# Performance work log

Measured on AMD Instinct MI355X. Metric: run time of the kernel, lower is better.

Reference implementation:

```python
import jax, jax.numpy as jnp
import numpy as np

B, L, H, I = 2, 2048, 4096, 11008


def setup_inputs() -> dict:
    key = jax.random.key(0)
    k1, k2, k3, k4, k5 = jax.random.split(key, 5)
    s_h = 1.0 / np.sqrt(H)
    s_i = 1.0 / np.sqrt(I)
    return {
        "hidden_states": jax.random.normal(k1, (B, L, H), dtype=jnp.float32),
        "w_up": jax.random.normal(k2, (I, H), dtype=jnp.float32) * s_h,
        "w_gate": jax.random.normal(k3, (I, H), dtype=jnp.float32) * s_h,
        "w_down": jax.random.normal(k4, (H, I), dtype=jnp.float32) * s_i,
        "route_mask": jax.random.randint(k5, (B, L), 0, 2, dtype=jnp.int32),
    }


def reference(hidden_states, w_up, w_gate, w_down, route_mask):
    # M-axis (per-token) route-masked gated MLP (SwiGLU, no biases).
    # up/gate: [B,L,H] @ [H,I] -> [B,L,I]; down: [B,L,I] @ [I,H] -> [B,L,H]
    up = jnp.einsum("blh,ih->bli", hidden_states, w_up)
    gate = jax.nn.silu(jnp.einsum("blh,ih->bli", hidden_states, w_gate))
    m = route_mask.astype(hidden_states.dtype)[..., None]  # [B,L,1]
    h = up * gate * m  # masked tokens contribute zero (down has no bias)
    return jnp.einsum("bli,hi->blh", h, w_down)
```

## Files before the change

kernel.cpp:

```cpp
#include <hip/hip_runtime.h>
#include <stdint.h>

#define MB_ 2
#define LL_ 2048
#define M_ (MB_*LL_)
#define H_ 4096
#define I_ 11008

typedef __attribute__((ext_vector_type(8))) short bf16x8;
typedef __attribute__((ext_vector_type(4))) float f32x4;
typedef __attribute__((ext_vector_type(4))) unsigned short us4;

__device__ __forceinline__ unsigned short f2bf(float f) {
  union { float f; unsigned int u; } v; v.f = f;
  unsigned int r = v.u + 0x7FFFu + ((v.u >> 16) & 1u);
  return (unsigned short)(r >> 16);
}

__device__ __forceinline__ void gl2lds16(const void* g, void* l) {
  __builtin_amdgcn_global_load_lds(
      (const __attribute__((address_space(1))) void*)g,
      (__attribute__((address_space(3))) void*)l, 16, 0, 0);
}

#define WAITV4 asm volatile("s_waitcnt vmcnt(4)" ::: "memory")
#define WAITV0 asm volatile("s_waitcnt vmcnt(0)" ::: "memory")
#define BAR    __builtin_amdgcn_s_barrier()

__global__ __launch_bounds__(256)
void compact_mask(const int* __restrict__ mask, int* __restrict__ idx,
                  int* __restrict__ cnt) {
  __shared__ int lcnt[256];
  __shared__ int loff[256];
  __shared__ int stot;
  const int t = threadIdx.x;
  const int base = t * 16;
  int c = 0;
#pragma unroll
  for (int j = 0; j < 16; j++) c += (mask[base + j] != 0);
  lcnt[t] = c;
  __syncthreads();
  if (t == 0) {
    int s = 0;
    for (int i = 0; i < 256; i++) { loff[i] = s; s += lcnt[i]; }
    stot = s;
    cnt[0] = s;
  }
  __syncthreads();
  int o = loff[t];
#pragma unroll
  for (int j = 0; j < 16; j++)
    if (mask[base + j] != 0) idx[o++] = base + j;
  const int total = stot;
  for (int s = total + t; s < M_; s += 256) idx[s] = 0;
}

__global__ __launch_bounds__(256)
void cvt_bf16(const float* __restrict__ src, unsigned short* __restrict__ dst, int n8) {
  int i = blockIdx.x * blockDim.x + threadIdx.x;
  if (i >= n8) return;
  const float4* s = (const float4*)src + (size_t)i * 2;
  float4 a = s[0], b = s[1];
  us4 lo = { f2bf(a.x), f2bf(a.y), f2bf(a.z), f2bf(a.w) };
  us4 hi = { f2bf(b.x), f2bf(b.y), f2bf(b.z), f2bf(b.w) };
  us4* d = (us4*)dst + (size_t)i * 2;
  d[0] = lo; d[1] = hi;
}

__global__ __launch_bounds__(256)
void gather_cvt_hs(const float* __restrict__ hs, const int* __restrict__ idx,
                   unsigned short* __restrict__ dst) {
  const int slot = blockIdx.x;
  const int row  = idx[slot];
  const int col  = (blockIdx.y * 256 + threadIdx.x) * 8;
  const float4* s = (const float4*)(hs + (size_t)row * H_ + col);
  float4 a = s[0], b = s[1];
  us4 lo = { f2bf(a.x), f2bf(a.y), f2bf(a.z), f2bf(a.w) };
  us4 hi = { f2bf(b.x), f2bf(b.y), f2bf(b.z), f2bf(b.w) };
  unsigned short* d = dst + (size_t)slot * H_ + col;
  *(us4*)d = lo;
  *(us4*)(d + 4) = hi;
}

__global__ __launch_bounds__(256)
void mlp_upgate3(const unsigned short* __restrict__ hs16c,
                 const unsigned short* __restrict__ wu16,
                 const unsigned short* __restrict__ wg16,
                 const int* __restrict__ cnt,
                 unsigned short* __restrict__ hbuf)
{
  const int mtiles = (cnt[0] + 127) >> 7;

  const int lin = blockIdx.y * 32 + blockIdx.x;
  const int sw  = (lin & 7) * 688 + (lin >> 3);
  const int mt  = sw & 31;
  const int nt  = sw >> 5;
  if (mt >= mtiles) return;

  __shared__ unsigned short As[3][128 * 32];
  __shared__ unsigned short Bu[3][64 * 32];
  __shared__ unsigned short Bg[3][64 * 32];

  const int tid  = threadIdx.x;
  const int m0   = mt * 128;
  const int n0   = nt * 64;
  const int w    = tid >> 6;
  const int lane = tid & 63;
  const int quad = lane >> 4;
  const int rrow = lane & 15;
  const int wm   = (w & 1) * 64;
  const int wn   = (w >> 1) * 32;

  const int lr = lane >> 2;
  const int lc = (lane & 3) * 8;
  const unsigned short* pa0 = hs16c + (size_t)(m0 + w * 32 + lr) * H_ + lc;
  const unsigned short* pa1 = pa0 + (size_t)16 * H_;
  const unsigned short* pu  = wu16 + (size_t)(n0 + w * 16 + lr) * H_ + lc;
  const unsigned short* pg  = wg16 + (size_t)(n0 + w * 16 + lr) * H_ + lc;

  auto stage = [&](int t, int b) {
    const int k0 = t * 32;
    gl2lds16(pa0 + k0, &As[b][(w * 32) * 32]);
    gl2lds16(pa1 + k0, &As[b][(w * 32 + 16) * 32]);
    gl2lds16(pu  + k0, &Bu[b][(w * 16) * 32]);
    gl2lds16(pg  + k0, &Bg[b][(w * 16) * 32]);
  };

  f32x4 accU[4][2], accG[4][2];
  const f32x4 zero = {0.f, 0.f, 0.f, 0.f};
  for (int i = 0; i < 4; i++)
    for (int j = 0; j < 2; j++) { accU[i][j] = zero; accG[i][j] = zero; }

  const int NT = H_ / 32;
  stage(0, 0);
  stage(1, 1);
  WAITV4;
  BAR;

  int b = 0, bs = 2;
  for (int t = 0; t < NT; ++t) {
    if (t + 2 < NT) stage(t + 2, bs);
    bf16x8 af[4], bu[2], bg[2];
#pragma unroll
    for (int mi = 0; mi < 4; mi++)
      af[mi] = *(const bf16x8*)&As[b][(wm + mi * 16 + rrow) * 32 + quad * 8];
#pragma unroll
    for (int ni = 0; ni < 2; ni++) {
      bu[ni] = *(const bf16x8*)&Bu[b][(wn + ni * 16 + rrow) * 32 + quad * 8];
      bg[ni] = *(const bf16x8*)&Bg[b][(wn + ni * 16 + rrow) * 32 + quad * 8];
    }
#pragma unroll
    for (int mi = 0; mi < 4; mi++)
#pragma unroll
      for (int ni = 0; ni < 2; ni++) {
        accU[mi][ni] = __builtin_amdgcn_mfma_f32_16x16x32_bf16(af[mi], bu[ni], accU[mi][ni], 0, 0, 0);
        accG[mi][ni] = __builtin_amdgcn_mfma_f32_16x16x32_bf16(af[mi], bg[ni], accG[mi][ni], 0, 0, 0);
      }
    if (t + 2 < NT) { WAITV4; } else { WAITV0; }
    BAR;
    b  = (b  + 1 == 3) ? 0 : b  + 1;
    bs = (bs + 1 == 3) ? 0 : bs + 1;
  }

#pragma unroll
  for (int mi = 0; mi < 4; mi++)
#pragma unroll
    for (int ni = 0; ni < 2; ni++)
#pragma unroll
      for (int r = 0; r < 4; r++) {
        int row = wm + mi * 16 + quad * 4 + r;
        int col = wn + ni * 16 + rrow;
        float u = accU[mi][ni][r];
        float g = accG[mi][ni][r];
        float sig = 1.0f / (1.0f + __expf(-g));
        hbuf[(size_t)(m0 + row) * I_ + n0 + col] = f2bf(u * g * sig);
      }
}

__global__ __launch_bounds__(256)
void mlp_down3(const unsigned short* __restrict__ hbuf,
               const unsigned short* __restrict__ wd16,
               const int* __restrict__ idx, const int* __restrict__ cnt,
               float* __restrict__ out)
{
  const int count  = cnt[0];
  const int mtiles = (count + 127) >> 7;

  const int lin = blockIdx.y * 32 + blockIdx.x;
  const int sw  = (lin & 7) * 128 + (lin >> 3);
  const int mt  = sw & 31;
  const int nt  = sw >> 5;
  if (mt >= mtiles) return;

  __shared__ unsigned short As[3][128 * 32];
  __shared__ unsigned short Bs[3][128 * 32];

  const int tid  = threadIdx.x;
  const int m0   = mt * 128;
  const int n0   = nt * 128;
  const int w    = tid >> 6;
  const int lane = tid & 63;
  const int quad = lane >> 4;
  const int rrow = lane & 15;
  const int wm   = (w & 1) * 64;
  const int wn   = (w >> 1) * 64;

  const int lr = lane >> 2;
  const int lc = (lane & 3) * 8;
  const unsigned short* pa0 = hbuf + (size_t)(m0 + w * 32 + lr) * I_ + lc;
  const unsigned short* pa1 = pa0 + (size_t)16 * I_;
  const unsigned short* pb0 = wd16 + (size_t)(n0 + w * 32 + lr) * I_ + lc;
  const unsigned short* pb1 = pb0 + (size_t)16 * I_;

  auto stage = [&](int t, int b) {
    const int k0 = t * 32;
    gl2lds16(pa0 + k0, &As[b][(w * 32) * 32]);
    gl2lds16(pa1 + k0, &As[b][(w * 32 + 16) * 32]);
    gl2lds16(pb0 + k0, &Bs[b][(w * 32) * 32]);
    gl2lds16(pb1 + k0, &Bs[b][(w * 32 + 16) * 32]);
  };

  f32x4 acc[4][4];
  const f32x4 zero = {0.f, 0.f, 0.f, 0.f};
  for (int i = 0; i < 4; i++)
    for (int j = 0; j < 4; j++) acc[i][j] = zero;

  const int NT = I_ / 32;
  stage(0, 0);
  stage(1, 1);
  WAITV4;
  BAR;

  int b = 0, bs = 2;
  for (int t = 0; t < NT; ++t) {
    if (t + 2 < NT) stage(t + 2, bs);
    bf16x8 af[4], bf[4];
#pragma unroll
    for (int mi = 0; mi < 4; mi++)
      af[mi] = *(const bf16x8*)&As[b][(wm + mi * 16 + rrow) * 32 + quad * 8];
#pragma unroll
    for (int ni = 0; ni < 4; ni++)
      bf[ni] = *(const bf16x8*)&Bs[b][(wn + ni * 16 + rrow) * 32 + quad * 8];
#pragma unroll
    for (int mi = 0; mi < 4; mi++)
#pragma unroll
      for (int ni = 0; ni < 4; ni++)
        acc[mi][ni] = __builtin_amdgcn_mfma_f32_16x16x32_bf16(af[mi], bf[ni], acc[mi][ni], 0, 0, 0);
    if (t + 2 < NT) { WAITV4; } else { WAITV0; }
    BAR;
    b  = (b  + 1 == 3) ? 0 : b  + 1;
    bs = (bs + 1 == 3) ? 0 : bs + 1;
  }

#pragma unroll
  for (int mi = 0; mi < 4; mi++)
#pragma unroll
    for (int r = 0; r < 4; r++) {
      int row  = wm + mi * 16 + quad * 4 + r;
      int slot = m0 + row;
      if (slot < count) {
        int tok = idx[slot];
        float* orow = out + (size_t)tok * H_ + n0;
#pragma unroll
        for (int ni = 0; ni < 4; ni++)
          orow[wn + ni * 16 + rrow] = acc[mi][ni][r];
      }
    }
}

#define TM 128
#define TN 128
#define BK 32
#define LDK 40

__global__ __launch_bounds__(256)
void mlp_upgate_fb(const float* __restrict__ hs, const float* __restrict__ wu,
                   const float* __restrict__ wg, const int* __restrict__ mask,
                   unsigned short* __restrict__ hbuf)
{
  __shared__ unsigned short As[TM * LDK];
  __shared__ unsigned short Bu[TN * LDK];
  __shared__ unsigned short Bg[TN * LDK];
  __shared__ float smask[TM];

  const int tid = threadIdx.x;
  const int m0 = blockIdx.x * TM;
  const int n0 = blockIdx.y * TN;
  if (tid < TM) smask[tid] = (float)mask[m0 + tid];
  const int wave = tid >> 6, lane = tid & 63;
  const int quad = lane >> 4, rrow = lane & 15;
  const int wm = (wave & 1) * 64, wn = (wave >> 1) * 64;

  f32x4 accU[4][4], accG[4][4];
  const f32x4 zero = {0.f, 0.f, 0.f, 0.f};
  for (int i = 0; i < 4; i++)
    for (int j = 0; j < 4; j++) { accU[i][j] = zero; accG[i][j] = zero; }

  for (int k0 = 0; k0 < H_; k0 += BK) {
#pragma unroll
    for (int s = 0; s < 4; s++) {
      int idx2 = tid + s * 256, row = idx2 >> 3, c4 = (idx2 & 7) * 4;
      float4 a = *(const float4*)&hs[(size_t)(m0 + row) * H_ + k0 + c4];
      float4 u = *(const float4*)&wu[(size_t)(n0 + row) * H_ + k0 + c4];
      float4 g = *(const float4*)&wg[(size_t)(n0 + row) * H_ + k0 + c4];
      us4 av = { f2bf(a.x), f2bf(a.y), f2bf(a.z), f2bf(a.w) };
      us4 uv = { f2bf(u.x), f2bf(u.y), f2bf(u.z), f2bf(u.w) };
      us4 gv = { f2bf(g.x), f2bf(g.y), f2bf(g.z), f2bf(g.w) };
      *(us4*)&As[row * LDK + c4] = av;
      *(us4*)&Bu[row * LDK + c4] = uv;
      *(us4*)&Bg[row * LDK + c4] = gv;
    }
    __syncthreads();
    bf16x8 af[4], bu[4], bg[4];
#pragma unroll
    for (int mi = 0; mi < 4; mi++)
      af[mi] = *(const bf16x8*)&As[(wm + mi * 16 + rrow) * LDK + quad * 8];
#pragma unroll
    for (int ni = 0; ni < 4; ni++) {
      bu[ni] = *(const bf16x8*)&Bu[(wn + ni * 16 + rrow) * LDK + quad * 8];
      bg[ni] = *(const bf16x8*)&Bg[(wn + ni * 16 + rrow) * LDK + quad * 8];
    }
#pragma unroll
    for (int mi = 0; mi < 4; mi++)
#pragma unroll
      for (int ni = 0; ni < 4; ni++) {
        accU[mi][ni] = __builtin_amdgcn_mfma_f32_16x16x32_bf16(af[mi], bu[ni], accU[mi][ni], 0, 0, 0);
        accG[mi][ni] = __builtin_amdgcn_mfma_f32_16x16x32_bf16(af[mi], bg[ni], accG[mi][ni], 0, 0, 0);
      }
    __syncthreads();
  }
#pragma unroll
  for (int mi = 0; mi < 4; mi++)
#pragma unroll
    for (int ni = 0; ni < 4; ni++)
#pragma unroll
      for (int r = 0; r < 4; r++) {
        int row = wm + mi * 16 + quad * 4 + r;
        int col = wn + ni * 16 + rrow;
        float u = accU[mi][ni][r], g = accG[mi][ni][r];
        float sig = 1.0f / (1.0f + __expf(-g));
        hbuf[(size_t)(m0 + row) * I_ + n0 + col] = f2bf(u * g * sig * smask[row]);
      }
}

__global__ __launch_bounds__(256)
void mlp_down_fb(const unsigned short* __restrict__ hbuf,
                 const float* __restrict__ wd, float* __restrict__ out)
{
  __shared__ unsigned short As[TM * LDK];
  __shared__ unsigned short Bs[TN * LDK];
  const int tid = threadIdx.x;
  const int m0 = blockIdx.x * TM, n0 = blockIdx.y * TN;
  const int wave = tid >> 6, lane = tid & 63;
  const int quad = lane >> 4, rrow = lane & 15;
  const int wm = (wave & 1) * 64, wn = (wave >> 1) * 64;

  f32x4 acc[4][4];
  const f32x4 zero = {0.f, 0.f, 0.f, 0.f};
  for (int i = 0; i < 4; i++)
    for (int j = 0; j < 4; j++) acc[i][j] = zero;

  for (int k0 = 0; k0 < I_; k0 += BK) {
#pragma unroll
    for (int s = 0; s < 4; s++) {
      int idx2 = tid + s * 256, row = idx2 >> 3, c4 = (idx2 & 7) * 4;
      us4 av = *(const us4*)&hbuf[(size_t)(m0 + row) * I_ + k0 + c4];
      float4 b = *(const float4*)&wd[(size_t)(n0 + row) * I_ + k0 + c4];
      us4 bv = { f2bf(b.x), f2bf(b.y), f2bf(b.z), f2bf(b.w) };
      *(us4*)&As[row * LDK + c4] = av;
      *(us4*)&Bs[row * LDK + c4] = bv;
    }
    __syncthreads();
    bf16x8 af[4], bf[4];
#pragma unroll
    for (int mi = 0; mi < 4; mi++)
      af[mi] = *(const bf16x8*)&As[(wm + mi * 16 + rrow) * LDK + quad * 8];
#pragma unroll
    for (int ni = 0; ni < 4; ni++)
      bf[ni] = *(const bf16x8*)&Bs[(wn + ni * 16 + rrow) * LDK + quad * 8];
#pragma unroll
    for (int mi = 0; mi < 4; mi++)
#pragma unroll
      for (int ni = 0; ni < 4; ni++)
        acc[mi][ni] = __builtin_amdgcn_mfma_f32_16x16x32_bf16(af[mi], bf[ni], acc[mi][ni], 0, 0, 0);
    __syncthreads();
  }
#pragma unroll
  for (int mi = 0; mi < 4; mi++)
#pragma unroll
    for (int ni = 0; ni < 4; ni++)
#pragma unroll
      for (int r = 0; r < 4; r++) {
        int row = wm + mi * 16 + quad * 4 + r;
        int col = wn + ni * 16 + rrow;
        out[(size_t)(m0 + row) * H_ + n0 + col] = acc[mi][ni][r];
      }
}

extern "C" void kernel_launch(void* const* d_in, const int* in_sizes, int n_in,
                              void* d_out, int out_size, void* d_ws, size_t ws_size,
                              hipStream_t stream) {
  const float* hs  = (const float*)d_in[0];
  const float* wu  = (const float*)d_in[1];
  const float* wg  = (const float*)d_in[2];
  const float* wd  = (const float*)d_in[3];
  const int*   msk = (const int*)d_in[4];
  float* out = (float*)d_out;

  const size_t SZ_H  = (size_t)M_ * I_ * 2;
  const size_t SZ_HS = (size_t)M_ * H_ * 2;
  const size_t SZ_W  = (size_t)I_ * H_ * 2;
  const size_t SZ_IDX = (size_t)M_ * 4 + 64;
  const size_t NEED = SZ_H + SZ_HS + 3 * SZ_W + SZ_IDX;

  unsigned short* hbuf = (unsigned short*)d_ws;

  if (ws_size >= NEED) {
    char* p = (char*)d_ws;
    unsigned short* hs16c = (unsigned short*)(p + SZ_H);
    unsigned short* wu16  = (unsigned short*)(p + SZ_H + SZ_HS);
    unsigned short* wg16  = (unsigned short*)(p + SZ_H + SZ_HS + SZ_W);
    unsigned short* wd16  = (unsigned short*)(p + SZ_H + SZ_HS + 2 * SZ_W);
    int* idx = (int*)(p + SZ_H + SZ_HS + 3 * SZ_W);
    int* cnt = idx + M_;

    hipMemsetAsync(out, 0, (size_t)out_size * sizeof(float), stream);

    compact_mask<<<1, 256, 0, stream>>>(msk, idx, cnt);
    gather_cvt_hs<<<dim3(M_, H_ / 2048), 256, 0, stream>>>(hs, idx, hs16c);

    const int n8_w = (int)((size_t)I_ * H_ / 8);
    cvt_bf16<<<(n8_w + 255) / 256, 256, 0, stream>>>(wu, wu16, n8_w);
    cvt_bf16<<<(n8_w + 255) / 256, 256, 0, stream>>>(wg, wg16, n8_w);
    cvt_bf16<<<(n8_w + 255) / 256, 256, 0, stream>>>(wd, wd16, n8_w);

    dim3 g1(M_ / 128, I_ / 64);
    mlp_upgate3<<<g1, dim3(256), 0, stream>>>(hs16c, wu16, wg16, cnt, hbuf);

    dim3 g2(M_ / 128, H_ / 128);
    mlp_down3<<<g2, dim3(256), 0, stream>>>(hbuf, wd16, idx, cnt, out);
  } else {
    dim3 g1(M_ / TM, I_ / TN);
    mlp_upgate_fb<<<g1, dim3(256), 0, stream>>>(hs, wu, wg, msk, hbuf);
    dim3 g2(M_ / TM, H_ / TN);
    mlp_down_fb<<<g2, dim3(256), 0, stream>>>(hbuf, wd, out);
  }
}
```

Before: 1.396 ms.

## Use 8-wave 128x256 tiles with BK=64, XOR-swizzled LDS and split-phase pipeline

Both GEMM kernels move to 512-thread blocks with larger output tiles (128x256 in the weight dimension, or 128x128 up plus 128 gate columns interleaved), a K step of 64 and an XOR swizzle on LDS rows to avoid bank conflicts. Each K step is split into two phases: the global-to-LDS prefetch is issued in halves and interleaved with the MFMA work, and wave priority is raised around the MFMA bursts. This is meant to raise arithmetic intensity, reduce LDS bank conflicts and barrier overhead per FLOP, and improve overlap of loads with MFMA. The cost is much more LDS per block (one block per CU), more barriers per iteration, and higher register pressure.

```diff
diff --git a/kernel.cpp b/kernel.cpp
--- a/kernel.cpp
+++ b/kernel.cpp
@@ -23,8 +23,9 @@
       (__attribute__((address_space(3))) void*)l, 16, 0, 0);
 }
 
-#define WAITV4 asm volatile("s_waitcnt vmcnt(4)" ::: "memory")
+#define WAITV6 asm volatile("s_waitcnt vmcnt(6)" ::: "memory")
 #define WAITV0 asm volatile("s_waitcnt vmcnt(0)" ::: "memory")
+#define LGKM0  asm volatile("s_waitcnt lgkmcnt(0)" ::: "memory")
 #define BAR    __builtin_amdgcn_s_barrier()
 
 __global__ __launch_bounds__(256)
@@ -82,8 +83,8 @@
   *(us4*)(d + 4) = hi;
 }
 
-__global__ __launch_bounds__(256)
-void mlp_upgate3(const unsigned short* __restrict__ hs16c,
+__global__ __launch_bounds__(512, 1)
+void mlp_upgate8(const unsigned short* __restrict__ hs16c,
                  const unsigned short* __restrict__ wu16,
                  const unsigned short* __restrict__ wg16,
                  const int* __restrict__ cnt,
@@ -92,72 +93,138 @@
   const int mtiles = (cnt[0] + 127) >> 7;
 
   const int lin = blockIdx.y * 32 + blockIdx.x;
-  const int sw  = (lin & 7) * 688 + (lin >> 3);
+  const int sw  = (lin & 7) * 344 + (lin >> 3);
   const int mt  = sw & 31;
   const int nt  = sw >> 5;
   if (mt >= mtiles) return;
 
-  __shared__ unsigned short As[3][128 * 32];
-  __shared__ unsigned short Bu[3][64 * 32];
-  __shared__ unsigned short Bg[3][64 * 32];
+  __shared__ unsigned short As[3][128 * 64];
+  __shared__ unsigned short Bs[3][256 * 64];
 
   const int tid  = threadIdx.x;
-  const int m0   = mt * 128;
-  const int n0   = nt * 64;
   const int w    = tid >> 6;
   const int lane = tid & 63;
   const int quad = lane >> 4;
   const int rrow = lane & 15;
-  const int wm   = (w & 1) * 64;
-  const int wn   = (w >> 1) * 32;
-
-  const int lr = lane >> 2;
-  const int lc = (lane & 3) * 8;
-  const unsigned short* pa0 = hs16c + (size_t)(m0 + w * 32 + lr) * H_ + lc;
-  const unsigned short* pa1 = pa0 + (size_t)16 * H_;
-  const unsigned short* pu  = wu16 + (size_t)(n0 + w * 16 + lr) * H_ + lc;
-  const unsigned short* pg  = wg16 + (size_t)(n0 + w * 16 + lr) * H_ + lc;
-
-  auto stage = [&](int t, int b) {
-    const int k0 = t * 32;
-    gl2lds16(pa0 + k0, &As[b][(w * 32) * 32]);
-    gl2lds16(pa1 + k0, &As[b][(w * 32 + 16) * 32]);
-    gl2lds16(pu  + k0, &Bu[b][(w * 16) * 32]);
-    gl2lds16(pg  + k0, &Bg[b][(w * 16) * 32]);
+  const int r7   = rrow & 7;
+  const int wr   = w >> 2;
+  const int wc   = w & 3;
+  const int m0   = mt * 128;
+  const int n0   = nt * 128;
+
+  const int cA0 = tid, cA1 = 512 + tid;
+  const int rA0 = cA0 >> 3, rA1 = cA1 >> 3;
+  const unsigned short* srcA0 =
+      hs16c + (size_t)(m0 + rA0) * H_ + (((cA0 & 7) ^ (rA0 & 7)) * 8);
+  const unsigned short* srcA1 =
+      hs16c + (size_t)(m0 + rA1) * H_ + (((cA1 & 7) ^ (rA1 & 7)) * 8);
+  const unsigned short* srcB[4];
+#pragma unroll
+  for (int j = 0; j < 4; j++) {
+    int c = j * 512 + tid;
+    int rowb = c >> 3;
+    int g = rowb >> 6, wi = rowb & 63;
+    const unsigned short* wb = (wi < 32) ? wu16 : wg16;
+    int grow = nt * 128 + g * 32 + (wi & 31);
+    srcB[j] = wb + (size_t)grow * H_ + (((c & 7) ^ (rowb & 7)) * 8);
+  }
+
+  auto stP1 = [&](int k0, int bb) {
+    gl2lds16(srcA0 + k0, &As[bb][cA0 * 8]);
+    gl2lds16(srcA1 + k0, &As[bb][cA1 * 8]);
+    gl2lds16(srcB[0] + k0, &Bs[bb][(0 * 512 + tid) * 8]);
+    gl2lds16(srcB[1] + k0, &Bs[bb][(1 * 512 + tid) * 8]);
   };
+  auto stP2 = [&](int k0, int bb) {
+    gl2lds16(srcB[2] + k0, &Bs[bb][(2 * 512 + tid) * 8]);
+    gl2lds16(srcB[3] + k0, &Bs[bb][(3 * 512 + tid) * 8]);
+  };
+
+  int aoff[4][2], buoff[2][2], bgoff[2][2];
+#pragma unroll
+  for (int mi = 0; mi < 4; mi++)
+#pragma unroll
+    for (int ks = 0; ks < 2; ks++) {
+      int row = wr * 64 + mi * 16 + rrow;
+      aoff[mi][ks] = row * 64 + (((ks * 4 + quad) ^ r7) * 8);
+    }
+#pragma unroll
+  for (int ni = 0; ni < 2; ni++)
+#pragma unroll
+    for (int ks = 0; ks < 2; ks++) {
+      int rowu = wc * 64 + ni * 16 + rrow;
+      int cs   = ((ks * 4 + quad) ^ r7) * 8;
+      buoff[ni][ks] = rowu * 64 + cs;
+      bgoff[ni][ks] = (rowu + 32) * 64 + cs;
+    }
 
   f32x4 accU[4][2], accG[4][2];
   const f32x4 zero = {0.f, 0.f, 0.f, 0.f};
+#pragma unroll
   for (int i = 0; i < 4; i++)
+#pragma unroll
     for (int j = 0; j < 2; j++) { accU[i][j] = zero; accG[i][j] = zero; }
 
-  const int NT = H_ / 32;
-  stage(0, 0);
-  stage(1, 1);
-  WAITV4;
+  const int NT = H_ / 64;
+  stP1(0, 0); stP2(0, 0);
+  stP1(64, 1); stP2(64, 1);
+  WAITV6;
   BAR;
 
   int b = 0, bs = 2;
   for (int t = 0; t < NT; ++t) {
-    if (t + 2 < NT) stage(t + 2, bs);
-    bf16x8 af[4], bu[2], bg[2];
-#pragma unroll
-    for (int mi = 0; mi < 4; mi++)
-      af[mi] = *(const bf16x8*)&As[b][(wm + mi * 16 + rrow) * 32 + quad * 8];
-#pragma unroll
-    for (int ni = 0; ni < 2; ni++) {
-      bu[ni] = *(const bf16x8*)&Bu[b][(wn + ni * 16 + rrow) * 32 + quad * 8];
-      bg[ni] = *(const bf16x8*)&Bg[b][(wn + ni * 16 + rrow) * 32 + quad * 8];
-    }
-#pragma unroll
-    for (int mi = 0; mi < 4; mi++)
-#pragma unroll
-      for (int ni = 0; ni < 2; ni++) {
-        accU[mi][ni] = __builtin_amdgcn_mfma_f32_16x16x32_bf16(af[mi], bu[ni], accU[mi][ni], 0, 0, 0);
-        accG[mi][ni] = __builtin_amdgcn_mfma_f32_16x16x32_bf16(af[mi], bg[ni], accG[mi][ni], 0, 0, 0);
-      }
-    if (t + 2 < NT) { WAITV4; } else { WAITV0; }
-    BAR;
+    bf16x8 bu2[2][2], bg2[2][2];
+    {
+      bf16x8 af[2][2];
+#pragma unroll
+      for (int mm = 0; mm < 2; mm++)
+#pragma unroll
+        for (int ks = 0; ks < 2; ks++)
+          af[mm][ks] = *(const bf16x8*)&As[b][aoff[mm][ks]];
+#pragma unroll
+      for (int ni = 0; ni < 2; ni++)
+#pragma unroll
+        for (int ks = 0; ks < 2; ks++) {
+          bu2[ni][ks] = *(const bf16x8*)&Bs[b][buoff[ni][ks]];
+          bg2[ni][ks] = *(const bf16x8*)&Bs[b][bgoff[ni][ks]];
+        }
+      if (t + 2 < NT) stP1((t + 2) * 64, bs);
+      BAR; LGKM0;
+      __builtin_amdgcn_s_setprio(1);
+#pragma unroll
+      for (int mm = 0; mm < 2; mm++)
+#pragma unroll
+        for (int ni = 0; ni < 2; ni++)
+#pragma unroll
+          for (int ks = 0; ks < 2; ks++) {
+            accU[mm][ni] = __builtin_amdgcn_mfma_f32_16x16x32_bf16(af[mm][ks], bu2[ni][ks], accU[mm][ni], 0, 0, 0);
+            accG[mm][ni] = __builtin_amdgcn_mfma_f32_16x16x32_bf16(af[mm][ks], bg2[ni][ks], accG[mm][ni], 0, 0, 0);
+          }
+      __builtin_amdgcn_s_setprio(0);
+      BAR;
+    }
+    {
+      bf16x8 af[2][2];
+#pragma unroll
+      for (int mm = 0; mm < 2; mm++)
+#pragma unroll
+        for (int ks = 0; ks < 2; ks++)
+          af[mm][ks] = *(const bf16x8*)&As[b][aoff[2 + mm][ks]];
+      if (t + 2 < NT) { stP2((t + 2) * 64, bs); WAITV6; } else { WAITV0; }
+      BAR; LGKM0;
+      __builtin_amdgcn_s_setprio(1);
+#pragma unroll
+      for (int mm = 0; mm < 2; mm++)
+#pragma unroll
+        for (int ni = 0; ni < 2; ni++)
+#pragma unroll
+          for (int ks = 0; ks < 2; ks++) {
+            accU[2 + mm][ni] = __builtin_amdgcn_mfma_f32_16x16x32_bf16(af[mm][ks], bu2[ni][ks], accU[2 + mm][ni], 0, 0, 0);
+            accG[2 + mm][ni] = __builtin_amdgcn_mfma_f32_16x16x32_bf16(af[mm][ks], bg2[ni][ks], accG[2 + mm][ni], 0, 0, 0);
+          }
+      __builtin_amdgcn_s_setprio(0);
+      BAR;
+    }
     b  = (b  + 1 == 3) ? 0 : b  + 1;
     bs = (bs + 1 == 3) ? 0 : bs + 1;
   }
@@ -168,8 +235,8 @@
     for (int ni = 0; ni < 2; ni++)
 #pragma unroll
       for (int r = 0; r < 4; r++) {
-        int row = wm + mi * 16 + quad * 4 + r;
-        int col = wn + ni * 16 + rrow;
+        int row = wr * 64 + mi * 16 + quad * 4 + r;
+        int col = wc * 32 + ni * 16 + rrow;
         float u = accU[mi][ni][r];
         float g = accG[mi][ni][r];
         float sig = 1.0f / (1.0f + __expf(-g));
@@ -177,8 +244,8 @@
       }
 }
 
-__global__ __launch_bounds__(256)
-void mlp_down3(const unsigned short* __restrict__ hbuf,
+__global__ __launch_bounds__(512, 1)
+void mlp_down8(const unsigned short* __restrict__ hbuf,
                const unsigned short* __restrict__ wd16,
                const int* __restrict__ idx, const int* __restrict__ cnt,
                float* __restrict__ out)
@@ -187,67 +254,127 @@
   const int mtiles = (count + 127) >> 7;
 
   const int lin = blockIdx.y * 32 + blockIdx.x;
-  const int sw  = (lin & 7) * 128 + (lin >> 3);
+  const int sw  = (lin & 7) * 64 + (lin >> 3);
   const int mt  = sw & 31;
   const int nt  = sw >> 5;
   if (mt >= mtiles) return;
 
-  __shared__ unsigned short As[3][128 * 32];
-  __shared__ unsigned short Bs[3][128 * 32];
+  __shared__ unsigned short As[3][128 * 64];
+  __shared__ unsigned short Bs[3][256 * 64];
 
   const int tid  = threadIdx.x;
-  const int m0   = mt * 128;
-  const int n0   = nt * 128;
   const int w    = tid >> 6;
   const int lane = tid & 63;
   const int quad = lane >> 4;
   const int rrow = lane & 15;
-  const int wm   = (w & 1) * 64;
-  const int wn   = (w >> 1) * 64;
-
-  const int lr = lane >> 2;
-  const int lc = (lane & 3) * 8;
-  const unsigned short* pa0 = hbuf + (size_t)(m0 + w * 32 + lr) * I_ + lc;
-  const unsigned short* pa1 = pa0 + (size_t)16 * I_;
-  const unsigned short* pb0 = wd16 + (size_t)(n0 + w * 32 + lr) * I_ + lc;
-  const unsigned short* pb1 = pb0 + (size_t)16 * I_;
-
-  auto stage = [&](int t, int b) {
-    const int k0 = t * 32;
-    gl2lds16(pa0 + k0, &As[b][(w * 32) * 32]);
-    gl2lds16(pa1 + k0, &As[b][(w * 32 + 16) * 32]);
-    gl2lds16(pb0 + k0, &Bs[b][(w * 32) * 32]);
-    gl2lds16(pb1 + k0, &Bs[b][(w * 32 + 16) * 32]);
+  const int r7   = rrow & 7;
+  const int wr   = w >> 2;
+  const int wc   = w & 3;
+  const int m0   = mt * 128;
+  const int n0   = nt * 256;
+
+  const int cA0 = tid, cA1 = 512 + tid;
+  const int rA0 = cA0 >> 3, rA1 = cA1 >> 3;
+  const unsigned short* srcA0 =
+      hbuf + (size_t)(m0 + rA0) * I_ + (((cA0 & 7) ^ (rA0 & 7)) * 8);
+  const unsigned short* srcA1 =
+      hbuf + (size_t)(m0 + rA1) * I_ + (((cA1 & 7) ^ (rA1 & 7)) * 8);
+  const unsigned short* srcB[4];
+#pragma unroll
+  for (int j = 0; j < 4; j++) {
+    int c = j * 512 + tid;
+    int rowb = c >> 3;
+    srcB[j] = wd16 + (size_t)(n0 + rowb) * I_ + (((c & 7) ^ (rowb & 7)) * 8);
+  }
+
+  auto stP1 = [&](int k0, int bb) {
+    gl2lds16(srcA0 + k0, &As[bb][cA0 * 8]);
+    gl2lds16(srcA1 + k0, &As[bb][cA1 * 8]);
+    gl2lds16(srcB[0] + k0, &Bs[bb][(0 * 512 + tid) * 8]);
+    gl2lds16(srcB[1] + k0, &Bs[bb][(1 * 512 + tid) * 8]);
   };
+  auto stP2 = [&](int k0, int bb) {
+    gl2lds16(srcB[2] + k0, &Bs[bb][(2 * 512 + tid) * 8]);
+    gl2lds16(srcB[3] + k0, &Bs[bb][(3 * 512 + tid) * 8]);
+  };
+
+  int aoff[4][2], boff[4][2];
+#pragma unroll
+  for (int mi = 0; mi < 4; mi++)
+#pragma unroll
+    for (int ks = 0; ks < 2; ks++) {
+      int row = wr * 64 + mi * 16 + rrow;
+      aoff[mi][ks] = row * 64 + (((ks * 4 + quad) ^ r7) * 8);
+    }
+#pragma unroll
+  for (int ni = 0; ni < 4; ni++)
+#pragma unroll
+    for (int ks = 0; ks < 2; ks++) {
+      int row = wc * 64 + ni * 16 + rrow;
+      boff[ni][ks] = row * 64 + (((ks * 4 + quad) ^ r7) * 8);
+    }
 
   f32x4 acc[4][4];
   const f32x4 zero = {0.f, 0.f, 0.f, 0.f};
+#pragma unroll
   for (int i = 0; i < 4; i++)
+#pragma unroll
     for (int j = 0; j < 4; j++) acc[i][j] = zero;
 
-  const int NT = I_ / 32;
-  stage(0, 0);
-  stage(1, 1);
-  WAITV4;
+  const int NT = I_ / 64;
+  stP1(0, 0); stP2(0, 0);
+  stP1(64, 1); stP2(64, 1);
+  WAITV6;
   BAR;
 
   int b = 0, bs = 2;
   for (int t = 0; t < NT; ++t) {
-    if (t + 2 < NT) stage(t + 2, bs);
-    bf16x8 af[4], bf[4];
-#pragma unroll
-    for (int mi = 0; mi < 4; mi++)
-      af[mi] = *(const bf16x8*)&As[b][(wm + mi * 16 + rrow) * 32 + quad * 8];
-#pragma unroll
-    for (int ni = 0; ni < 4; ni++)
-      bf[ni] = *(const bf16x8*)&Bs[b][(wn + ni * 16 + rrow) * 32 + quad * 8];
-#pragma unroll
-    for (int mi = 0; mi < 4; mi++)
+    bf16x8 bf2[4][2];
+    {
+      bf16x8 af[2][2];
+#pragma unroll
+      for (int mm = 0; mm < 2; mm++)
+#pragma unroll
+        for (int ks = 0; ks < 2; ks++)
+          af[mm][ks] = *(const bf16x8*)&As[b][aoff[mm][ks]];
 #pragma unroll
       for (int ni = 0; ni < 4; ni++)
-        acc[mi][ni] = __builtin_amdgcn_mfma_f32_16x16x32_bf16(af[mi], bf[ni], acc[mi][ni], 0, 0, 0);
-    if (t + 2 < NT) { WAITV4; } else { WAITV0; }
-    BAR;
+#pragma unroll
+        for (int ks = 0; ks < 2; ks++)
+          bf2[ni][ks] = *(const bf16x8*)&Bs[b][boff[ni][ks]];
+      if (t + 2 < NT) stP1((t + 2) * 64, bs);
+      BAR; LGKM0;
+      __builtin_amdgcn_s_setprio(1);
+#pragma unroll
+      for (int mm = 0; mm < 2; mm++)
+#pragma unroll
+        for (int ni = 0; ni < 4; ni++)
+#pragma unroll
+          for (int ks = 0; ks < 2; ks++)
+            acc[mm][ni] = __builtin_amdgcn_mfma_f32_16x16x32_bf16(af[mm][ks], bf2[ni][ks], acc[mm][ni], 0, 0, 0);
+      __builtin_amdgcn_s_setprio(0);
+      BAR;
+    }
+    {
+      bf16x8 af[2][2];
+#pragma unroll
+      for (int mm = 0; mm < 2; mm++)
+#pragma unroll
+        for (int ks = 0; ks < 2; ks++)
+          af[mm][ks] = *(const bf16x8*)&As[b][aoff[2 + mm][ks]];
+      if (t + 2 < NT) { stP2((t + 2) * 64, bs); WAITV6; } else { WAITV0; }
+      BAR; LGKM0;
+      __builtin_amdgcn_s_setprio(1);
+#pragma unroll
+      for (int mm = 0; mm < 2; mm++)
+#pragma unroll
+        for (int ni = 0; ni < 4; ni++)
+#pragma unroll
+          for (int ks = 0; ks < 2; ks++)
+            acc[2 + mm][ni] = __builtin_amdgcn_mfma_f32_16x16x32_bf16(af[mm][ks], bf2[ni][ks], acc[2 + mm][ni], 0, 0, 0);
+      __builtin_amdgcn_s_setprio(0);
+      BAR;
+    }
     b  = (b  + 1 == 3) ? 0 : b  + 1;
     bs = (bs + 1 == 3) ? 0 : bs + 1;
   }
@@ -256,14 +383,14 @@
   for (int mi = 0; mi < 4; mi++)
 #pragma unroll
     for (int r = 0; r < 4; r++) {
-      int row  = wm + mi * 16 + quad * 4 + r;
+      int row  = wr * 64 + mi * 16 + quad * 4 + r;
       int slot = m0 + row;
       if (slot < count) {
         int tok = idx[slot];
         float* orow = out + (size_t)tok * H_ + n0;
 #pragma unroll
         for (int ni = 0; ni < 4; ni++)
-          orow[wn + ni * 16 + rrow] = acc[mi][ni][r];
+          orow[wc * 64 + ni * 16 + rrow] = acc[mi][ni][r];
       }
     }
 }
@@ -434,11 +561,11 @@
     cvt_bf16<<<(n8_w + 255) / 256, 256, 0, stream>>>(wg, wg16, n8_w);
     cvt_bf16<<<(n8_w + 255) / 256, 256, 0, stream>>>(wd, wd16, n8_w);
 
-    dim3 g1(M_ / 128, I_ / 64);
-    mlp_upgate3<<<g1, dim3(256), 0, stream>>>(hs16c, wu16, wg16, cnt, hbuf);
-
-    dim3 g2(M_ / 128, H_ / 128);
-    mlp_down3<<<g2, dim3(256), 0, stream>>>(hbuf, wd16, idx, cnt, out);
+    dim3 g1(32, I_ / 128);
+    mlp_upgate8<<<g1, dim3(512), 0, stream>>>(hs16c, wu16, wg16, cnt, hbuf);
+
+    dim3 g2(32, H_ / 256);
+    mlp_down8<<<g2, dim3(512), 0, stream>>>(hbuf, wd16, idx, cnt, out);
   } else {
     dim3 g1(M_ / TM, I_ / TN);
     mlp_upgate_fb<<<g1, dim3(256), 0, stream>>>(hs, wu, wg, msk, hbuf);
```

Result: faster. 1.280 ms (-8.3%).
